# Performance work log

Measured on AMD Instinct MI355X. Metric: run time of the kernel, lower is better.

## Reference

```python
import jax, jax.numpy as jnp
import numpy as np


def setup_inputs() -> dict:
    key = jax.random.key(0)
    k1, k2 = jax.random.split(key)
    B, S_ENC, S_DEC, D = 8, 2048, 2048, 1024
    enc_outputs = jax.random.normal(k1, (B, S_ENC, D), dtype=jnp.float32)
    dec_outputs = jax.random.normal(k2, (B, S_DEC, D), dtype=jnp.float32)
    return {"enc_outputs": enc_outputs, "dec_outputs": dec_outputs}


def reference(enc_outputs, dec_outputs):
    # scores: [B, S_enc, S_dec] = enc @ dec^T (unscaled)
    a_t = jnp.einsum('bed,btd->bet', enc_outputs, dec_outputs)
    a_t = jax.nn.softmax(a_t, axis=-1)
    # context: [B, S_dec, D] = a_t^T @ enc
    c_t = jnp.einsum('bet,bed->btd', a_t, enc_outputs)
    return c_t
```

## Files before the change

### kernel.cpp

```cpp
#include <hip/hip_runtime.h>


typedef _Float16 half8 __attribute__((ext_vector_type(8)));
typedef _Float16 half4v __attribute__((ext_vector_type(4)));
typedef float floatx4 __attribute__((ext_vector_type(4)));

__device__ __forceinline__ void async_load16(const _Float16* g, void* l) {
  __builtin_amdgcn_global_load_lds(
      (const __attribute__((address_space(1))) void*)g,
      (__attribute__((address_space(3))) void*)l, 16, 0, 0);
}

template <typename OutT>
__global__ __launch_bounds__(512, 2) void gemm8p(
    const _Float16* __restrict__ A, const _Float16* __restrict__ Bt,
    OutT* __restrict__ C, int K, long strideA, long strideB, long strideC,
    int ldA, int ldB, int ldC) {
  extern __shared__ char smem_[];
  const int tid = threadIdx.x;
  const int lane = tid & 63;
  const int wave = tid >> 6;
  const int wm = wave >> 2;
  const int wn = wave & 3;
  const int l15 = lane & 15;
  const int lh = lane >> 4;

  const int gx = gridDim.x, gxy = gridDim.x * gridDim.y;
  int fid = blockIdx.z * gxy + blockIdx.y * gx + blockIdx.x;
  const int nwg = gxy * gridDim.z;
  fid = (fid & 7) * (nwg >> 3) + (fid >> 3);
  const int b = fid / gxy;
  const int rem = fid - b * gxy;
  const int m0 = (rem / gx) * 256;
  const int n0 = (rem % gx) * 256;

  A += (long)b * strideA + (long)m0 * ldA;
  Bt += (long)b * strideB + (long)n0 * ldB;
  C += (long)b * strideC;

  const int lb0 = l15 * 128 + ((lh ^ (l15 & 7)) << 4);
  const int lb1 = lb0 ^ 64;
  const char* aBuf[2] = {smem_ + wm * 16384, smem_ + 32768 + wm * 16384};
  const char* bBuf[2] = {
      smem_ + 65536 + (wn >> 1) * 16384 + (wn & 1) * 8192,
      smem_ + 98304 + (wn >> 1) * 16384 + (wn & 1) * 8192};
  char* aSlot[2] = {smem_, smem_ + 32768};
  char* bSlot[2] = {smem_ + 65536, smem_ + 98304};

  const int srow = tid >> 3;
  const int skk = ((tid & 7) ^ (srow & 7)) << 3;
  const _Float16* Ast = A + (long)srow * ldA + skk;
  const _Float16* Bst = Bt + (long)srow * ldB + skk;
  const int dst = tid << 4;

  floatx4 acc[8][4] = {};
  half8 a[4][2], b0[2][2], b1[2][2];

  auto stage = [&](const _Float16* gs, int ld, int k0, char* slot) {
#pragma unroll
    for (int i = 0; i < 4; ++i)
      async_load16(gs + (long)(i * 64) * ld + k0, slot + i * 8192 + dst);
  };
  auto mm = [&](int mh, int nh, half8(&bb)[2][2]) {
    __builtin_amdgcn_s_setprio(1);
#pragma unroll
    for (int s = 0; s < 2; ++s)
#pragma unroll
      for (int q = 0; q < 4; ++q)
#pragma unroll
        for (int n = 0; n < 2; ++n)
          acc[mh * 4 + q][nh * 2 + n] = __builtin_amdgcn_mfma_f32_16x16x32_f16(
              a[q][s], bb[n][s], acc[mh * 4 + q][nh * 2 + n], 0, 0, 0);
    __builtin_amdgcn_s_setprio(0);
  };
  auto bar = [&]() { asm volatile("s_barrier" ::: "memory"); };

  auto quad4 = [&](int cur, int kst, bool last) {
    const char* aB_ = aBuf[cur];
    const char* bB_ = bBuf[cur];
#pragma unroll
    for (int q = 0; q < 4; ++q) {
      a[q][0] = *(const half8*)(aB_ + lb0 + q * 2048);
      a[q][1] = *(const half8*)(aB_ + lb1 + q * 2048);
    }
#pragma unroll
    for (int n = 0; n < 2; ++n) {
      b0[n][0] = *(const half8*)(bB_ + lb0 + n * 2048);
      b0[n][1] = *(const half8*)(bB_ + lb1 + n * 2048);
      b1[n][0] = *(const half8*)(bB_ + lb0 + (n + 2) * 2048);
      b1[n][1] = *(const half8*)(bB_ + lb1 + (n + 2) * 2048);
    }
    bar();
    mm(0, 0, b0);
    bar();
    bar();
    mm(0, 1, b1);
    bar();
#pragma unroll
    for (int q = 0; q < 4; ++q) {
      a[q][0] = *(const half8*)(aB_ + lb0 + (q + 4) * 2048);
      a[q][1] = *(const half8*)(aB_ + lb1 + (q + 4) * 2048);
    }
    if (kst >= 0) stage(Bst, ldB, kst, bSlot[cur]);
    bar();
    mm(1, 1, b1);
    bar();
    if (kst >= 0) stage(Ast, ldA, kst, aSlot[cur]);
    mm(1, 0, b0);
    if (last)
      asm volatile("s_waitcnt vmcnt(0)" ::: "memory");
    else
      asm volatile("s_waitcnt vmcnt(8)" ::: "memory");
    bar();
  };

  stage(Ast, ldA, 0, aSlot[0]);
  stage(Bst, ldB, 0, bSlot[0]);
  stage(Ast, ldA, 64, aSlot[1]);
  stage(Bst, ldB, 64, bSlot[1]);
  asm volatile("s_waitcnt vmcnt(8)" ::: "memory");
  bar();

  const int NT = K >> 6;
  for (int i = 0; i < (NT >> 1) - 1; ++i) {
    quad4(0, (2 * i + 2) * 64, false);
    quad4(1, (2 * i + 3) * 64, false);
  }
  quad4(0, -1, true);
  quad4(1, -1, true);

#pragma unroll
  for (int mf = 0; mf < 8; ++mf) {
    const long r0 = (long)(m0 + wm * 128 + mf * 16 + lh * 4);
#pragma unroll
    for (int nf = 0; nf < 4; ++nf) {
      const int cc = n0 + wn * 64 + nf * 16 + l15;
#pragma unroll
      for (int rr = 0; rr < 4; ++rr)
        C[(r0 + rr) * ldC + cc] = (OutT)acc[mf][nf][rr];
    }
  }
}

__global__ __launch_bounds__(256) void conv_enc(const float* __restrict__ E,
                                                _Float16* __restrict__ Eh,
                                                _Float16* __restrict__ EhT,
                                                int Se, int D) {
  __shared__ _Float16 T[64][72];
  const int b = blockIdx.z;
  const int d0 = blockIdx.x * 64;
  const int e0 = blockIdx.y * 64;
  const float* Eb = E + (size_t)b * Se * D;
  _Float16* Ehb = Eh + (size_t)b * Se * D;
  _Float16* EhTb = EhT + (size_t)b * D * Se;
  const int tid = threadIdx.x;
  const int tx = tid & 15;
  const int ty = tid >> 4;

  half4v h[4];
#pragma unroll
  for (int r = 0; r < 4; ++r) {
    const int e = e0 + ty * 4 + r;
    float4 v = *(const float4*)(Eb + (size_t)e * D + d0 + tx * 4);
    h[r][0] = (_Float16)v.x; h[r][1] = (_Float16)v.y;
    h[r][2] = (_Float16)v.z; h[r][3] = (_Float16)v.w;
    *(half4v*)(Ehb + (size_t)e * D + d0 + tx * 4) = h[r];
  }
#pragma unroll
  for (int c = 0; c < 4; ++c) {
    half4v w;
#pragma unroll
    for (int r = 0; r < 4; ++r) w[r] = h[r][c];
    *(half4v*)&T[tx * 4 + c][ty * 4] = w;
  }
  __syncthreads();
#pragma unroll
  for (int p = 0; p < 2; ++p) {
    const int idx = tid + p * 256;
    const int row = idx >> 3;
    const int ck = idx & 7;
    *(half8*)(EhTb + (size_t)(d0 + row) * Se + e0 + ck * 8) =
        *(const half8*)&T[row][ck * 8];
  }
}

__global__ __launch_bounds__(256) void conv_dec(const float* __restrict__ X,
                                                _Float16* __restrict__ Y) {
  const size_t i = ((size_t)blockIdx.x * 256 + threadIdx.x) * 8;
  float4 a = *(const float4*)(X + i);
  float4 b = *(const float4*)(X + i + 4);
  half8 h;
  h[0] = (_Float16)a.x; h[1] = (_Float16)a.y;
  h[2] = (_Float16)a.z; h[3] = (_Float16)a.w;
  h[4] = (_Float16)b.x; h[5] = (_Float16)b.y;
  h[6] = (_Float16)b.z; h[7] = (_Float16)b.w;
  *(half8*)(Y + i) = h;
}

__global__ __launch_bounds__(256) void col_stats(const _Float16* __restrict__ ST,
                                                 float2* __restrict__ part) {
  __shared__ float2 red[16][65];
  const int b = blockIdx.z;
  const int e0 = blockIdx.x * 64;
  const int t0 = blockIdx.y * 512;
  const _Float16* S = ST + (size_t)b * 2048 * 2048;
  const int tx = threadIdx.x & 15;
  const int ty = threadIdx.x >> 4;

  float m[4] = {-1e30f, -1e30f, -1e30f, -1e30f};
  float s[4] = {0.f, 0.f, 0.f, 0.f};
  for (int it = 0; it < 32; ++it) {
    const int t = t0 + it * 16 + ty;
    half4v v = *(const half4v*)(S + (size_t)t * 2048 + e0 + tx * 4);
#pragma unroll
    for (int c = 0; c < 4; ++c) {
      const float x = (float)v[c];
      const float m2 = fmaxf(m[c], x);
      s[c] = s[c] * __expf(m[c] - m2) + __expf(x - m2);
      m[c] = m2;
    }
  }
#pragma unroll
  for (int c = 0; c < 4; ++c) red[ty][tx * 4 + c] = make_float2(m[c], s[c]);
  __syncthreads();
  if (threadIdx.x < 64) {
    float2 a = red[0][threadIdx.x];
#pragma unroll
    for (int r = 1; r < 16; ++r) {
      const float2 o = red[r][threadIdx.x];
      const float m2 = fmaxf(a.x, o.x);
      a.y = a.y * __expf(a.x - m2) + o.y * __expf(o.x - m2);
      a.x = m2;
    }
    part[(size_t)blockIdx.y * 16384 + (size_t)b * 2048 + e0 + threadIdx.x] = a;
  }
}

__global__ __launch_bounds__(256) void stats_combine(
    const float2* __restrict__ part, float2* __restrict__ stats) {
  const int idx = blockIdx.x * 256 + threadIdx.x;
  float2 a = part[idx];
#pragma unroll
  for (int tc = 1; tc < 4; ++tc) {
    const float2 o = part[tc * 16384 + idx];
    const float m2 = fmaxf(a.x, o.x);
    a.y = a.y * __expf(a.x - m2) + o.y * __expf(o.x - m2);
    a.x = m2;
  }
  stats[idx] = make_float2(a.x, 1.0f / a.y);
}

__global__ __launch_bounds__(256) void norm_stream(
    const _Float16* __restrict__ ST, const float2* __restrict__ stats,
    _Float16* __restrict__ P) {
  const int b = blockIdx.y;
  const int t0 = blockIdx.x * 4;
  const int e = threadIdx.x * 8;
  float m_[8], rl_[8];
#pragma unroll
  for (int j = 0; j < 8; ++j) {
    const float2 st = stats[(size_t)b * 2048 + e + j];
    m_[j] = st.x;
    rl_[j] = st.y;
  }
  const size_t base = ((size_t)b * 2048 + t0) * 2048 + e;
#pragma unroll
  for (int r = 0; r < 4; ++r) {
    half8 v = *(const half8*)(ST + base + (size_t)r * 2048);
    half8 o;
#pragma unroll
    for (int j = 0; j < 8; ++j)
      o[j] = (_Float16)(__expf((float)v[j] - m_[j]) * rl_[j]);
    *(half8*)(P + base + (size_t)r * 2048) = o;
  }
}

extern "C" void kernel_launch(void* const* d_in, const int* in_sizes, int n_in,
                              void* d_out, int out_size, void* d_ws,
                              size_t ws_size, hipStream_t stream) {
  const float* enc = (const float*)d_in[0];
  const float* dec = (const float*)d_in[1];
  float* out = (float*)d_out;

  const int B = 8, SE = 2048, SD = 2048, D = 1024;
  char* ws = (char*)d_ws;
  _Float16* enc_h = (_Float16*)ws;
  _Float16* dec_h = (_Float16*)(ws + 33554432);
  _Float16* P = (_Float16*)ws;
  _Float16* enc_hT = (_Float16*)(ws + 67108864);
  _Float16* ST = (_Float16*)(ws + 100663296);
  float2* stats = (float2*)(ws + 167772160);
  float2* part = (float2*)(ws + 167903232);

  static int smem_set = 0;
  if (!smem_set) {
    (void)hipFuncSetAttribute(
        reinterpret_cast<const void*>(&gemm8p<_Float16>),
        hipFuncAttributeMaxDynamicSharedMemorySize, 131072);
    (void)hipFuncSetAttribute(
        reinterpret_cast<const void*>(&gemm8p<float>),
        hipFuncAttributeMaxDynamicSharedMemorySize, 131072);
    smem_set = 1;
  }

  conv_enc<<<dim3(D / 64, SE / 64, B), 256, 0, stream>>>(enc, enc_h, enc_hT,
                                                         SE, D);
  conv_dec<<<dim3((size_t)B * SD * D / 2048), 256, 0, stream>>>(dec, dec_h);
  gemm8p<_Float16><<<dim3(SE / 256, SD / 256, B), 512, 131072, stream>>>(
      dec_h, enc_h, ST, D, (long)SD * D, (long)SE * D, (long)SD * SE, D, D,
      SE);
  col_stats<<<dim3(32, 4, B), 256, 0, stream>>>(ST, part);
  stats_combine<<<dim3(64), 256, 0, stream>>>(part, stats);
  norm_stream<<<dim3(512, B), 256, 0, stream>>>(ST, stats, P);
  gemm8p<float><<<dim3(D / 256, SD / 256, B), 512, 131072, stream>>>(
      P, enc_hT, out, SE, (long)SD * SE, (long)D * SE, (long)SD * D, SE, SE,
      D);
}
```

Baseline: 332.0 us.

## Fuse column softmax stats into score GEMM and normalization into context GEMM

The first GEMM now computes per-column max/sum partials from its fp16-rounded accumulators in its epilogue, which replaces the separate col_stats pass over the score matrix. The second GEMM loads raw scores through registers, applies exp and normalization on the fly, and writes the result into LDS, which removes the norm_stream kernel and the materialized P buffer. This saves two full read passes and one write pass over the 64MB score matrix. The cost is that the A-operand path in the second GEMM changes from async direct-to-LDS loads to register-staged loads with exp math, which adds VALU work and raises register pressure inside the pipelined loop.

Result: slower. 425.1 us (+28.0%).

```diff
diff --git a/kernel.cpp b/kernel.cpp
--- a/kernel.cpp
+++ b/kernel.cpp
@@ -11,11 +11,12 @@
       (__attribute__((address_space(3))) void*)l, 16, 0, 0);
 }
 
-template <typename OutT>
+template <typename OutT, bool NORM, bool STATS>
 __global__ __launch_bounds__(512, 2) void gemm8p(
     const _Float16* __restrict__ A, const _Float16* __restrict__ Bt,
-    OutT* __restrict__ C, int K, long strideA, long strideB, long strideC,
-    int ldA, int ldB, int ldC) {
+    OutT* __restrict__ C, const float2* __restrict__ st_in,
+    float2* __restrict__ part_out, int K, long strideA, long strideB,
+    long strideC, int ldA, int ldB, int ldC) {
   extern __shared__ char smem_[];
   const int tid = threadIdx.x;
   const int lane = tid & 63;
@@ -37,6 +38,7 @@
   A += (long)b * strideA + (long)m0 * ldA;
   Bt += (long)b * strideB + (long)n0 * ldB;
   C += (long)b * strideC;
+  const float2* statsB = NORM ? st_in + (size_t)b * 2048 : nullptr;
 
   const int lb0 = l15 * 128 + ((lh ^ (l15 & 7)) << 4);
   const int lb1 = lb0 ^ 64;
@@ -51,6 +53,8 @@
   const int skk = ((tid & 7) ^ (srow & 7)) << 3;
   const _Float16* Ast = A + (long)srow * ldA + skk;
   const _Float16* Bst = Bt + (long)srow * ldB + skk;
+  const _Float16* AstN = A + (long)srow * ldA + ((tid & 7) << 3);
+  const int awOff = (srow << 7) + (((tid & 7) ^ (srow & 7)) << 4);
   const int dst = tid << 4;
 
   floatx4 acc[8][4] = {};
@@ -78,6 +82,8 @@
   auto quad4 = [&](int cur, int kst, bool last) {
     const char* aB_ = aBuf[cur];
     const char* bB_ = bBuf[cur];
+    half8 stg[4];
+    float4 f0_, f1_, f2_, f3_;
 #pragma unroll
     for (int q = 0; q < 4; ++q) {
       a[q][0] = *(const half8*)(aB_ + lb0 + q * 2048);
@@ -101,25 +107,82 @@
       a[q][0] = *(const half8*)(aB_ + lb0 + (q + 4) * 2048);
       a[q][1] = *(const half8*)(aB_ + lb1 + (q + 4) * 2048);
     }
-    if (kst >= 0) stage(Bst, ldB, kst, bSlot[cur]);
+    if (kst >= 0) {
+      if constexpr (NORM) {
+        const float4* sp = (const float4*)(statsB + kst + ((tid & 7) << 3));
+        f0_ = sp[0]; f1_ = sp[1]; f2_ = sp[2]; f3_ = sp[3];
+#pragma unroll
+        for (int i = 0; i < 4; ++i)
+          stg[i] = *(const half8*)(AstN + (long)(i * 64) * ldA + kst);
+      }
+      stage(Bst, ldB, kst, bSlot[cur]);
+    }
     bar();
     mm(1, 1, b1);
     bar();
-    if (kst >= 0) stage(Ast, ldA, kst, aSlot[cur]);
-    mm(1, 0, b0);
-    if (last)
-      asm volatile("s_waitcnt vmcnt(0)" ::: "memory");
-    else
-      asm volatile("s_waitcnt vmcnt(8)" ::: "memory");
-    bar();
+    if constexpr (NORM) {
+      if (kst >= 0) {
+        const float em[8] = {f0_.x, f0_.z, f1_.x, f1_.z,
+                             f2_.x, f2_.z, f3_.x, f3_.z};
+        const float er[8] = {f0_.y, f0_.w, f1_.y, f1_.w,
+                             f2_.y, f2_.w, f3_.y, f3_.w};
+#pragma unroll
+        for (int i = 0; i < 4; ++i) {
+          half8 v = stg[i];
+          half8 o;
+#pragma unroll
+          for (int j = 0; j < 8; ++j)
+            o[j] = (_Float16)(__expf((float)v[j] - em[j]) * er[j]);
+          *(half8*)(aSlot[cur] + i * 8192 + awOff) = o;
+        }
+        mm(1, 0, b0);
+        asm volatile("s_waitcnt lgkmcnt(0)" ::: "memory");
+      } else {
+        mm(1, 0, b0);
+        asm volatile("s_waitcnt vmcnt(0)" ::: "memory");
+      }
+      bar();
+    } else {
+      if (kst >= 0) stage(Ast, ldA, kst, aSlot[cur]);
+      mm(1, 0, b0);
+      if (last)
+        asm volatile("s_waitcnt vmcnt(0)" ::: "memory");
+      else
+        asm volatile("s_waitcnt vmcnt(8)" ::: "memory");
+      bar();
+    }
   };
 
-  stage(Ast, ldA, 0, aSlot[0]);
-  stage(Bst, ldB, 0, bSlot[0]);
-  stage(Ast, ldA, 64, aSlot[1]);
-  stage(Bst, ldB, 64, bSlot[1]);
-  asm volatile("s_waitcnt vmcnt(8)" ::: "memory");
-  bar();
+  if constexpr (NORM) {
+    stage(Bst, ldB, 0, bSlot[0]);
+    stage(Bst, ldB, 64, bSlot[1]);
+#pragma unroll
+    for (int t = 0; t < 2; ++t) {
+      const int k0 = t * 64;
+      const float4* sp = (const float4*)(statsB + k0 + ((tid & 7) << 3));
+      float4 f0 = sp[0], f1 = sp[1], f2 = sp[2], f3 = sp[3];
+      const float em[8] = {f0.x, f0.z, f1.x, f1.z, f2.x, f2.z, f3.x, f3.z};
+      const float er[8] = {f0.y, f0.w, f1.y, f1.w, f2.y, f2.w, f3.y, f3.w};
+#pragma unroll
+      for (int i = 0; i < 4; ++i) {
+        half8 v = *(const half8*)(AstN + (long)(i * 64) * ldA + k0);
+        half8 o;
+#pragma unroll
+        for (int j = 0; j < 8; ++j)
+          o[j] = (_Float16)(__expf((float)v[j] - em[j]) * er[j]);
+        *(half8*)(aSlot[t] + i * 8192 + awOff) = o;
+      }
+    }
+    asm volatile("s_waitcnt vmcnt(4) lgkmcnt(0)" ::: "memory");
+    bar();
+  } else {
+    stage(Ast, ldA, 0, aSlot[0]);
+    stage(Bst, ldB, 0, bSlot[0]);
+    stage(Ast, ldA, 64, aSlot[1]);
+    stage(Bst, ldB, 64, bSlot[1]);
+    asm volatile("s_waitcnt vmcnt(8)" ::: "memory");
+    bar();
+  }
 
   const int NT = K >> 6;
   for (int i = 0; i < (NT >> 1) - 1; ++i) {
@@ -138,6 +201,47 @@
 #pragma unroll
       for (int rr = 0; rr < 4; ++rr)
         C[(r0 + rr) * ldC + cc] = (OutT)acc[mf][nf][rr];
+    }
+  }
+
+  if constexpr (STATS) {
+    float2* sm = (float2*)smem_;
+#pragma unroll
+    for (int nf = 0; nf < 4; ++nf) {
+      float x16[8][4];
+#pragma unroll
+      for (int mf = 0; mf < 8; ++mf)
+#pragma unroll
+        for (int rr = 0; rr < 4; ++rr)
+          x16[mf][rr] = (float)(_Float16)acc[mf][nf][rr];
+      float mx = -1e30f;
+#pragma unroll
+      for (int mf = 0; mf < 8; ++mf)
+#pragma unroll
+        for (int rr = 0; rr < 4; ++rr) mx = fmaxf(mx, x16[mf][rr]);
+      float ss = 0.f;
+#pragma unroll
+      for (int mf = 0; mf < 8; ++mf)
+#pragma unroll
+        for (int rr = 0; rr < 4; ++rr) ss += __expf(x16[mf][rr] - mx);
+#pragma unroll
+      for (int d = 16; d <= 32; d <<= 1) {
+        const float om = __shfl_xor(mx, d, 64);
+        const float os = __shfl_xor(ss, d, 64);
+        const float m2 = fmaxf(mx, om);
+        ss = ss * __expf(mx - m2) + os * __expf(om - m2);
+        mx = m2;
+      }
+      if (lh == 0) sm[wm * 256 + wn * 64 + nf * 16 + l15] = make_float2(mx, ss);
+    }
+    __syncthreads();
+    if (tid < 256) {
+      const float2 a0 = sm[tid], a1 = sm[256 + tid];
+      const float m2 = fmaxf(a0.x, a1.x);
+      const float s2 =
+          a0.y * __expf(a0.x - m2) + a1.y * __expf(a1.x - m2);
+      part_out[(size_t)(m0 >> 8) * 16384 + (size_t)b * 2048 + n0 + tid] =
+          make_float2(m2, s2);
     }
   }
 }
@@ -197,82 +301,18 @@
   *(half8*)(Y + i) = h;
 }
 
-__global__ __launch_bounds__(256) void col_stats(const _Float16* __restrict__ ST,
-                                                 float2* __restrict__ part) {
-  __shared__ float2 red[16][65];
-  const int b = blockIdx.z;
-  const int e0 = blockIdx.x * 64;
-  const int t0 = blockIdx.y * 512;
-  const _Float16* S = ST + (size_t)b * 2048 * 2048;
-  const int tx = threadIdx.x & 15;
-  const int ty = threadIdx.x >> 4;
-
-  float m[4] = {-1e30f, -1e30f, -1e30f, -1e30f};
-  float s[4] = {0.f, 0.f, 0.f, 0.f};
-  for (int it = 0; it < 32; ++it) {
-    const int t = t0 + it * 16 + ty;
-    half4v v = *(const half4v*)(S + (size_t)t * 2048 + e0 + tx * 4);
-#pragma unroll
-    for (int c = 0; c < 4; ++c) {
-      const float x = (float)v[c];
-      const float m2 = fmaxf(m[c], x);
-      s[c] = s[c] * __expf(m[c] - m2) + __expf(x - m2);
-      m[c] = m2;
-    }
-  }
-#pragma unroll
-  for (int c = 0; c < 4; ++c) red[ty][tx * 4 + c] = make_float2(m[c], s[c]);
-  __syncthreads();
-  if (threadIdx.x < 64) {
-    float2 a = red[0][threadIdx.x];
-#pragma unroll
-    for (int r = 1; r < 16; ++r) {
-      const float2 o = red[r][threadIdx.x];
-      const float m2 = fmaxf(a.x, o.x);
-      a.y = a.y * __expf(a.x - m2) + o.y * __expf(o.x - m2);
-      a.x = m2;
-    }
-    part[(size_t)blockIdx.y * 16384 + (size_t)b * 2048 + e0 + threadIdx.x] = a;
-  }
-}
-
 __global__ __launch_bounds__(256) void stats_combine(
     const float2* __restrict__ part, float2* __restrict__ stats) {
   const int idx = blockIdx.x * 256 + threadIdx.x;
   float2 a = part[idx];
 #pragma unroll
-  for (int tc = 1; tc < 4; ++tc) {
+  for (int tc = 1; tc < 8; ++tc) {
     const float2 o = part[tc * 16384 + idx];
     const float m2 = fmaxf(a.x, o.x);
     a.y = a.y * __expf(a.x - m2) + o.y * __expf(o.x - m2);
     a.x = m2;
   }
   stats[idx] = make_float2(a.x, 1.0f / a.y);
-}
-
-__global__ __launch_bounds__(256) void norm_stream(
-    const _Float16* __restrict__ ST, const float2* __restrict__ stats,
-    _Float16* __restrict__ P) {
-  const int b = blockIdx.y;
-  const int t0 = blockIdx.x * 4;
-  const int e = threadIdx.x * 8;
-  float m_[8], rl_[8];
-#pragma unroll
-  for (int j = 0; j < 8; ++j) {
-    const float2 st = stats[(size_t)b * 2048 + e + j];
-    m_[j] = st.x;
-    rl_[j] = st.y;
-  }
-  const size_t base = ((size_t)b * 2048 + t0) * 2048 + e;
-#pragma unroll
-  for (int r = 0; r < 4; ++r) {
-    half8 v = *(const half8*)(ST + base + (size_t)r * 2048);
-    half8 o;
-#pragma unroll
-    for (int j = 0; j < 8; ++j)
-      o[j] = (_Float16)(__expf((float)v[j] - m_[j]) * rl_[j]);
-    *(half8*)(P + base + (size_t)r * 2048) = o;
-  }
 }
 
 extern "C" void kernel_launch(void* const* d_in, const int* in_sizes, int n_in,
@@ -286,19 +326,18 @@
   char* ws = (char*)d_ws;
   _Float16* enc_h = (_Float16*)ws;
   _Float16* dec_h = (_Float16*)(ws + 33554432);
-  _Float16* P = (_Float16*)ws;
   _Float16* enc_hT = (_Float16*)(ws + 67108864);
   _Float16* ST = (_Float16*)(ws + 100663296);
   float2* stats = (float2*)(ws + 167772160);
-  float2* part = (float2*)(ws + 167903232);
+  float2* part2 = (float2*)(ws + 167903232);
 
   static int smem_set = 0;
   if (!smem_set) {
     (void)hipFuncSetAttribute(
-        reinterpret_cast<const void*>(&gemm8p<_Float16>),
+        reinterpret_cast<const void*>(&gemm8p<_Float16, false, true>),
         hipFuncAttributeMaxDynamicSharedMemorySize, 131072);
     (void)hipFuncSetAttribute(
-        reinterpret_cast<const void*>(&gemm8p<float>),
+        reinterpret_cast<const void*>(&gemm8p<float, true, false>),
         hipFuncAttributeMaxDynamicSharedMemorySize, 131072);
     smem_set = 1;
   }
@@ -306,13 +345,13 @@
   conv_enc<<<dim3(D / 64, SE / 64, B), 256, 0, stream>>>(enc, enc_h, enc_hT,
                                                          SE, D);
   conv_dec<<<dim3((size_t)B * SD * D / 2048), 256, 0, stream>>>(dec, dec_h);
-  gemm8p<_Float16><<<dim3(SE / 256, SD / 256, B), 512, 131072, stream>>>(
-      dec_h, enc_h, ST, D, (long)SD * D, (long)SE * D, (long)SD * SE, D, D,
-      SE);
-  col_stats<<<dim3(32, 4, B), 256, 0, stream>>>(ST, part);
-  stats_combine<<<dim3(64), 256, 0, stream>>>(part, stats);
-  norm_stream<<<dim3(512, B), 256, 0, stream>>>(ST, stats, P);
-  gemm8p<float><<<dim3(D / 256, SD / 256, B), 512, 131072, stream>>>(
-      P, enc_hT, out, SE, (long)SD * SE, (long)D * SE, (long)SD * D, SE, SE,
-      D);
-}
+  gemm8p<_Float16, false, true>
+      <<<dim3(SE / 256, SD / 256, B), 512, 131072, stream>>>(
+          dec_h, enc_h, ST, nullptr, part2, D, (long)SD * D, (long)SE * D,
+          (long)SD * SE, D, D, SE);
+  stats_combine<<<dim3(64), 256, 0, stream>>>(part2, stats);
+  gemm8p<float, true, false>
+      <<<dim3(D / 256, SD / 256, B), 512, 131072, stream>>>(
+          ST, enc_hT, out, stats, nullptr, SE, (long)SD * SE, (long)D * SE,
+          (long)SD * D, SE, SE, D);
+}
```
